# Kernel tuning notes

Measured on AMD Instinct MI355X. Metric: run time of the kernel, lower is better.

## Reference

```python
import jax, jax.numpy as jnp
import numpy as np

N_INPUTS = 1024
N_MIDDLE = 256
N_OUTPUTS = 64
BATCH = 65536


def setup_inputs() -> dict:
    key = jax.random.key(0)
    k_x, k_w1, k_w2 = jax.random.split(key, 3)
    x = jax.random.normal(k_x, (BATCH, N_INPUTS), dtype=jnp.float32)
    # Synapse weights k are initialized with random.random() in [0, 1)
    W1 = jax.random.uniform(k_w1, (N_MIDDLE, N_INPUTS), dtype=jnp.float32)
    W2 = jax.random.uniform(k_w2, (N_OUTPUTS, N_MIDDLE), dtype=jnp.float32)
    # Neuron biases b are initialized to 0.0
    b1 = jnp.zeros((N_MIDDLE,), dtype=jnp.float32)
    b2 = jnp.zeros((N_OUTPUTS,), dtype=jnp.float32)
    return {"x": x, "W1": W1, "b1": b1, "W2": W2, "b2": b2}


def reference(x, W1, b1, W2, b2):
    # Middle RegularNeurons: relu(sum_j k_ij * x_j + b_i)
    h = jax.nn.relu(jnp.einsum('bi,mi->bm', x, W1) + b1)  # [B, n_middle]
    # Output DestinationNeurons: relu(sum_m k_om * h_m + b_o)
    y = jax.nn.relu(jnp.einsum('bm,om->bo', h, W2) + b2)  # [B, n_outputs]
    return y
```

## Files before the change

kernel.cpp:

```cpp
#include <hip/hip_runtime.h>
#include <stdint.h>

#define NIN 1024
#define NMID 256
#define NOUT 64
#define BM 128
#define BK 64
#define NSTEP (NIN / BK)

typedef __attribute__((ext_vector_type(8))) short bf16x8;
typedef __attribute__((ext_vector_type(4))) float fx4;
typedef __attribute__((ext_vector_type(16))) float f32x16;
typedef __attribute__((ext_vector_type(4))) uint32_t u32x4;

#define XS_TILE 16384
#define W1_OFF  32768
#define W1_TILE 32768
#define LDS_SZ  98304

__device__ __forceinline__ uint32_t cvtpk(float lo, float hi) {
  uint32_t r;
  asm("v_cvt_pk_bf16_f32 %0, %1, %2" : "=v"(r) : "v"(lo), "v"(hi));
  return r;
}

__device__ __forceinline__ void gload16(const void* g, void* l) {
  __builtin_amdgcn_global_load_lds(
      (const __attribute__((address_space(1))) uint32_t*)g,
      (__attribute__((address_space(3))) uint32_t*)l, 16, 0, 0);
}

__global__ __launch_bounds__(256) void cvt_weights(
    const float* __restrict__ W1, const float* __restrict__ W2,
    unsigned short* __restrict__ w1b, unsigned short* __restrict__ w2b) {
  int e = (blockIdx.x * 256 + threadIdx.x) << 2;
  const int n1 = NMID * NIN;
  if (e < n1) {
    fx4 v = *(const fx4*)(W1 + e);
    uint2 p;
    p.x = cvtpk(v.x, v.y);
    p.y = cvtpk(v.z, v.w);
    *(uint2*)(w1b + e) = p;
  } else {
    int e2 = e - n1;
    if (e2 < NOUT * NMID) {
      fx4 v = *(const fx4*)(W2 + e2);
      uint2 p;
      p.x = cvtpk(v.x, v.y);
      p.y = cvtpk(v.z, v.w);
      *(uint2*)(w2b + e2) = p;
    }
  }
}

__global__ __launch_bounds__(512, 2) void livenet_main(
    const float* __restrict__ x,
    const unsigned short* __restrict__ w1b,
    const float* __restrict__ b1,
    const unsigned short* __restrict__ w2b,
    const float* __restrict__ b2,
    float* __restrict__ y) {

  extern __shared__ __align__(16) char smem[];

  const int tid = threadIdx.x;
  const int lane = tid & 63;
  const int w = tid >> 6;
  const int wm = w >> 2;
  const int wn = w & 3;
  const int l31 = lane & 31;
  const int lh = lane >> 5;
  const int row0 = blockIdx.x * BM;

  const int xr_row = tid >> 2;
  const int xr_c = tid & 3;
  const float* xbase = x + (size_t)(row0 + xr_row) * NIN + xr_c * 16;
  const int xrx = xr_row & 7;
  const uint32_t xd0 = (uint32_t)(xr_row * 128 + (((2 * xr_c) ^ xrx) << 4));
  const uint32_t xd1 = (uint32_t)(xr_row * 128 + (((2 * xr_c + 1) ^ xrx) << 4));

  uint32_t w1src[4], w1dst[4];
#pragma unroll
  for (int i = 0; i < 4; ++i) {
    uint32_t o = (uint32_t)(i * 8192 + tid * 16);
    uint32_t r = o >> 7;
    uint32_t pc = (o >> 4) & 7u;
    uint32_t j = pc ^ (r & 7u);
    w1src[i] = r * NIN + j * 8u;
    w1dst[i] = o;
  }

  fx4 xl[4];
#define XLOAD(k0)                                     \
  {                                                   \
    const float* p_ = xbase + (k0);                   \
    xl[0] = *(const fx4*)p_;                          \
    xl[1] = *(const fx4*)(p_ + 4);                    \
    xl[2] = *(const fx4*)(p_ + 8);                    \
    xl[3] = *(const fx4*)(p_ + 12);                   \
  }

#define XWRITE(buf)                                                   \
  {                                                                   \
    u32x4 A_ = {cvtpk(xl[0].x, xl[0].y), cvtpk(xl[0].z, xl[0].w),     \
                cvtpk(xl[1].x, xl[1].y), cvtpk(xl[1].z, xl[1].w)};    \
    u32x4 B_ = {cvtpk(xl[2].x, xl[2].y), cvtpk(xl[2].z, xl[2].w),     \
                cvtpk(xl[3].x, xl[3].y), cvtpk(xl[3].z, xl[3].w)};    \
    char* xb_ = smem + (buf) * XS_TILE;                               \
    *(u32x4*)(xb_ + xd0) = A_;                                        \
    *(u32x4*)(xb_ + xd1) = B_;                                        \
  }

#define W1STAGE(buf, k0)                                                      \
  {                                                                           \
    char* wb_ = smem + W1_OFF + (buf) * W1_TILE;                              \
    _Pragma("unroll") for (int i_ = 0; i_ < 4; ++i_)                          \
        gload16(w1b + w1src[i_] + (k0), wb_ + w1dst[i_]);                     \
  }

  f32x16 acc[2][2];
#pragma unroll
  for (int mt = 0; mt < 2; ++mt)
#pragma unroll
    for (int nt = 0; nt < 2; ++nt)
#pragma unroll
      for (int q = 0; q < 16; ++q) acc[mt][nt][q] = 0.f;

  W1STAGE(0, 0);
  XLOAD(0);
  XWRITE(0);
  __syncthreads();

  uint32_t aoff[2], boff[2];
#pragma unroll
  for (int mt = 0; mt < 2; ++mt) {
    uint32_t R = (uint32_t)(wm * 64 + mt * 32 + l31);
    aoff[mt] = R * 128u;
  }
#pragma unroll
  for (int nt = 0; nt < 2; ++nt) {
    uint32_t R = (uint32_t)(wn * 64 + nt * 32 + l31);
    boff[nt] = R * 128u;
  }
  const uint32_t arx0 = (uint32_t)((wm * 64 + l31) & 7);
  const uint32_t brx0 = (uint32_t)((wn * 64 + l31) & 7);

  for (int ks = 0; ks < NSTEP; ++ks) {
    const int cur = ks & 1, nxt = cur ^ 1;
    if (ks + 1 < NSTEP) {
      W1STAGE(nxt, (ks + 1) * BK);
      XLOAD((ks + 1) * BK);
    }

    char* xsb = smem + cur * XS_TILE;
    char* w1sb = smem + W1_OFF + cur * W1_TILE;

    bf16x8 a[2][4], b[2][4];
#pragma unroll
    for (int mt = 0; mt < 2; ++mt) {
      uint32_t rx = arx0;
#pragma unroll
      for (int kk = 0; kk < 4; ++kk)
        a[mt][kk] = *(const bf16x8*)(xsb + aoff[mt] +
                                     ((((uint32_t)(kk * 2 + lh)) ^ rx) << 4));
    }
#pragma unroll
    for (int nt = 0; nt < 2; ++nt) {
      uint32_t rx = brx0;
#pragma unroll
      for (int kk = 0; kk < 4; ++kk)
        b[nt][kk] = *(const bf16x8*)(w1sb + boff[nt] +
                                     ((((uint32_t)(kk * 2 + lh)) ^ rx) << 4));
    }

#pragma unroll
    for (int mt = 0; mt < 2; ++mt)
#pragma unroll
      for (int nt = 0; nt < 2; ++nt)
#pragma unroll
        for (int kk = 0; kk < 4; ++kk)
          acc[mt][nt] = __builtin_amdgcn_mfma_f32_32x32x16_bf16(
              a[mt][kk], b[nt][kk], acc[mt][nt], 0, 0, 0);

    if (ks + 1 < NSTEP) XWRITE(nxt);
    __syncthreads();
  }

  float b1v[2];
#pragma unroll
  for (int nt = 0; nt < 2; ++nt) b1v[nt] = b1[wn * 64 + nt * 32 + l31];

#pragma unroll
  for (int mt = 0; mt < 2; ++mt) {
#pragma unroll
    for (int nt = 0; nt < 2; ++nt) {
      int col = wn * 64 + nt * 32 + l31;
#pragma unroll
      for (int rg = 0; rg < 16; ++rg) {
        int row = wm * 64 + mt * 32 + (rg & 3) + 8 * (rg >> 2) + 4 * lh;
        float v = acc[mt][nt][rg] + b1v[nt];
        v = v > 0.f ? v : 0.f;
        int j = (col >> 3) ^ (row & 31);
        *(unsigned short*)(smem + row * 512 + (j << 4) + (col & 7) * 2) =
            (unsigned short)cvtpk(v, v);
      }
    }
  }
  __syncthreads();

  f32x16 acc2;
#pragma unroll
  for (int q = 0; q < 16; ++q) acc2[q] = 0.f;

  const int r2 = (w >> 1) * 32;
  const int c2 = (w & 1) * 32;
  const int arow = r2 + l31;
  const uint32_t arx = (uint32_t)(arow & 31);
  const unsigned short* w2row = w2b + (size_t)(c2 + l31) * NMID + lh * 8;

#pragma unroll
  for (int kk = 0; kk < 16; ++kk) {
    bf16x8 a2 = *(const bf16x8*)(smem + arow * 512 +
                                 ((((uint32_t)(kk * 2 + lh)) ^ arx) << 4));
    bf16x8 bw = *(const bf16x8*)(w2row + kk * 16);
    acc2 = __builtin_amdgcn_mfma_f32_32x32x16_bf16(a2, bw, acc2, 0, 0, 0);
  }

  float bias2 = b2[c2 + l31];
#pragma unroll
  for (int rg = 0; rg < 16; ++rg) {
    int row = r2 + (rg & 3) + 8 * (rg >> 2) + 4 * lh;
    float v = acc2[rg] + bias2;
    v = v > 0.f ? v : 0.f;
    y[(size_t)(row0 + row) * NOUT + c2 + l31] = v;
  }
}

extern "C" void kernel_launch(void* const* d_in, const int* in_sizes, int n_in,
                              void* d_out, int out_size, void* d_ws, size_t ws_size,
                              hipStream_t stream) {
  const float* x  = (const float*)d_in[0];
  const float* W1 = (const float*)d_in[1];
  const float* b1 = (const float*)d_in[2];
  const float* W2 = (const float*)d_in[3];
  const float* b2 = (const float*)d_in[4];
  float* y = (float*)d_out;

  unsigned short* w1b = (unsigned short*)d_ws;
  unsigned short* w2b = w1b + (size_t)NMID * NIN;

  const int batch = in_sizes[0] / NIN;

  const int tot4 = (NMID * NIN + NOUT * NMID) / 4;
  hipLaunchKernelGGL(cvt_weights, dim3((tot4 + 255) / 256), dim3(256), 0, stream,
                     W1, W2, w1b, w2b);

  static int lds_set = 0;
  if (!lds_set) {
    hipFuncSetAttribute((const void*)livenet_main,
                        hipFuncAttributeMaxDynamicSharedMemorySize, LDS_SZ);
    lds_set = 1;
  }
  hipLaunchKernelGGL(livenet_main, dim3(batch / BM), dim3(512), LDS_SZ, stream,
                     x, w1b, b1, w2b, b2, y);
}
```

Before: 81.86 us.

## Deepen x prefetch with manual vmcnt waits, raw barriers and MFMA priority

Restructures the K-loop so x global loads run two steps ahead in registers while the W1 direct-to-LDS loads run one step ahead. Generic __syncthreads is replaced by explicit s_waitcnt vmcnt/lgkmcnt plus s_barrier and sched_barrier fences, and the loop is peeled into a prologue, 14 steady iterations and an epilogue. s_setprio is raised around the MFMA block to favour matrix issue. The aim is to hide global load latency behind compute and avoid over-conservative waits. The hand-counted vmcnt values depend on load issue order, so a wrong count could race or stall.

```diff
diff --git a/kernel.cpp b/kernel.cpp
--- a/kernel.cpp
+++ b/kernel.cpp
@@ -6,7 +6,6 @@
 #define NOUT 64
 #define BM 128
 #define BK 64
-#define NSTEP (NIN / BK)
 
 typedef __attribute__((ext_vector_type(8))) short bf16x8;
 typedef __attribute__((ext_vector_type(4))) float fx4;
@@ -14,21 +13,26 @@
 typedef __attribute__((ext_vector_type(4))) uint32_t u32x4;
 
 #define XS_TILE 16384
-#define W1_OFF  32768
+#define WOFF    32768
 #define W1_TILE 32768
 #define LDS_SZ  98304
 
-__device__ __forceinline__ uint32_t cvtpk(float lo, float hi) {
+static __device__ __forceinline__ uint32_t cvtpk(float lo, float hi) {
   uint32_t r;
   asm("v_cvt_pk_bf16_f32 %0, %1, %2" : "=v"(r) : "v"(lo), "v"(hi));
   return r;
 }
-
-__device__ __forceinline__ void gload16(const void* g, void* l) {
+static __device__ __forceinline__ void gload16(const void* g, void* l) {
   __builtin_amdgcn_global_load_lds(
       (const __attribute__((address_space(1))) uint32_t*)g,
       (__attribute__((address_space(3))) uint32_t*)l, 16, 0, 0);
 }
+
+#define VMCNT4() asm volatile("s_waitcnt vmcnt(4)" ::: "memory")
+#define VMCNT0() asm volatile("s_waitcnt vmcnt(0)" ::: "memory")
+#define LGKM0()  asm volatile("s_waitcnt lgkmcnt(0)" ::: "memory")
+#define SBAR()   __builtin_amdgcn_s_barrier()
+#define SFENCE() __builtin_amdgcn_sched_barrier(0)
 
 __global__ __launch_bounds__(256) void cvt_weights(
     const float* __restrict__ W1, const float* __restrict__ W2,
@@ -37,17 +41,13 @@
   const int n1 = NMID * NIN;
   if (e < n1) {
     fx4 v = *(const fx4*)(W1 + e);
-    uint2 p;
-    p.x = cvtpk(v.x, v.y);
-    p.y = cvtpk(v.z, v.w);
+    uint2 p; p.x = cvtpk(v.x, v.y); p.y = cvtpk(v.z, v.w);
     *(uint2*)(w1b + e) = p;
   } else {
     int e2 = e - n1;
     if (e2 < NOUT * NMID) {
       fx4 v = *(const fx4*)(W2 + e2);
-      uint2 p;
-      p.x = cvtpk(v.x, v.y);
-      p.y = cvtpk(v.z, v.w);
+      uint2 p; p.x = cvtpk(v.x, v.y); p.y = cvtpk(v.z, v.w);
       *(uint2*)(w2b + e2) = p;
     }
   }
@@ -90,33 +90,27 @@
     w1dst[i] = o;
   }
 
-  fx4 xl[4];
-#define XLOAD(k0)                                     \
-  {                                                   \
-    const float* p_ = xbase + (k0);                   \
-    xl[0] = *(const fx4*)p_;                          \
-    xl[1] = *(const fx4*)(p_ + 4);                    \
-    xl[2] = *(const fx4*)(p_ + 8);                    \
-    xl[3] = *(const fx4*)(p_ + 12);                   \
-  }
-
-#define XWRITE(buf)                                                   \
-  {                                                                   \
-    u32x4 A_ = {cvtpk(xl[0].x, xl[0].y), cvtpk(xl[0].z, xl[0].w),     \
-                cvtpk(xl[1].x, xl[1].y), cvtpk(xl[1].z, xl[1].w)};    \
-    u32x4 B_ = {cvtpk(xl[2].x, xl[2].y), cvtpk(xl[2].z, xl[2].w),     \
-                cvtpk(xl[3].x, xl[3].y), cvtpk(xl[3].z, xl[3].w)};    \
-    char* xb_ = smem + (buf) * XS_TILE;                               \
+  fx4 xr[4];
+#define XLOAD(k0)                               \
+  { const float* p_ = xbase + (k0);             \
+    xr[0] = *(const fx4*)p_;                    \
+    xr[1] = *(const fx4*)(p_ + 4);              \
+    xr[2] = *(const fx4*)(p_ + 8);              \
+    xr[3] = *(const fx4*)(p_ + 12); }
+
+#define XWRITE(pbuf)                                                  \
+  { u32x4 A_ = {cvtpk(xr[0].x, xr[0].y), cvtpk(xr[0].z, xr[0].w),     \
+                cvtpk(xr[1].x, xr[1].y), cvtpk(xr[1].z, xr[1].w)};    \
+    u32x4 B_ = {cvtpk(xr[2].x, xr[2].y), cvtpk(xr[2].z, xr[2].w),     \
+                cvtpk(xr[3].x, xr[3].y), cvtpk(xr[3].z, xr[3].w)};    \
+    char* xb_ = smem + (pbuf) * XS_TILE;                              \
     *(u32x4*)(xb_ + xd0) = A_;                                        \
-    *(u32x4*)(xb_ + xd1) = B_;                                        \
-  }
-
-#define W1STAGE(buf, k0)                                                      \
-  {                                                                           \
-    char* wb_ = smem + W1_OFF + (buf) * W1_TILE;                              \
-    _Pragma("unroll") for (int i_ = 0; i_ < 4; ++i_)                          \
-        gload16(w1b + w1src[i_] + (k0), wb_ + w1dst[i_]);                     \
-  }
+    *(u32x4*)(xb_ + xd1) = B_; }
+
+#define W1STAGE(pbuf, k0)                                             \
+  { char* wb_ = smem + WOFF + (pbuf) * W1_TILE;                       \
+    _Pragma("unroll") for (int i_ = 0; i_ < 4; ++i_)                  \
+      gload16(w1b + w1src[i_] + (k0), wb_ + w1dst[i_]); }
 
   f32x16 acc[2][2];
 #pragma unroll
@@ -126,65 +120,80 @@
 #pragma unroll
       for (int q = 0; q < 16; ++q) acc[mt][nt][q] = 0.f;
 
-  W1STAGE(0, 0);
-  XLOAD(0);
-  XWRITE(0);
-  __syncthreads();
-
   uint32_t aoff[2], boff[2];
 #pragma unroll
-  for (int mt = 0; mt < 2; ++mt) {
-    uint32_t R = (uint32_t)(wm * 64 + mt * 32 + l31);
-    aoff[mt] = R * 128u;
-  }
-#pragma unroll
-  for (int nt = 0; nt < 2; ++nt) {
-    uint32_t R = (uint32_t)(wn * 64 + nt * 32 + l31);
-    boff[nt] = R * 128u;
-  }
+  for (int mt = 0; mt < 2; ++mt)
+    aoff[mt] = (uint32_t)(wm * 64 + mt * 32 + l31) * 128u;
+#pragma unroll
+  for (int nt = 0; nt < 2; ++nt)
+    boff[nt] = (uint32_t)(wn * 64 + nt * 32 + l31) * 128u;
   const uint32_t arx0 = (uint32_t)((wm * 64 + l31) & 7);
   const uint32_t brx0 = (uint32_t)((wn * 64 + l31) & 7);
 
-  for (int ks = 0; ks < NSTEP; ++ks) {
-    const int cur = ks & 1, nxt = cur ^ 1;
-    if (ks + 1 < NSTEP) {
-      W1STAGE(nxt, (ks + 1) * BK);
-      XLOAD((ks + 1) * BK);
-    }
-
-    char* xsb = smem + cur * XS_TILE;
-    char* w1sb = smem + W1_OFF + cur * W1_TILE;
-
-    bf16x8 a[2][4], b[2][4];
-#pragma unroll
-    for (int mt = 0; mt < 2; ++mt) {
-      uint32_t rx = arx0;
-#pragma unroll
-      for (int kk = 0; kk < 4; ++kk)
-        a[mt][kk] = *(const bf16x8*)(xsb + aoff[mt] +
-                                     ((((uint32_t)(kk * 2 + lh)) ^ rx) << 4));
-    }
-#pragma unroll
-    for (int nt = 0; nt < 2; ++nt) {
-      uint32_t rx = brx0;
-#pragma unroll
-      for (int kk = 0; kk < 4; ++kk)
-        b[nt][kk] = *(const bf16x8*)(w1sb + boff[nt] +
-                                     ((((uint32_t)(kk * 2 + lh)) ^ rx) << 4));
-    }
-
-#pragma unroll
-    for (int mt = 0; mt < 2; ++mt)
-#pragma unroll
-      for (int nt = 0; nt < 2; ++nt)
-#pragma unroll
-        for (int kk = 0; kk < 4; ++kk)
-          acc[mt][nt] = __builtin_amdgcn_mfma_f32_32x32x16_bf16(
-              a[mt][kk], b[nt][kk], acc[mt][nt], 0, 0, 0);
-
-    if (ks + 1 < NSTEP) XWRITE(nxt);
-    __syncthreads();
-  }
+#define STEP_COMPUTE(xb, wb)                                              \
+  { bf16x8 a[2][4], b[2][4];                                              \
+    _Pragma("unroll") for (int mt = 0; mt < 2; ++mt)                      \
+      _Pragma("unroll") for (int kk = 0; kk < 4; ++kk)                    \
+        a[mt][kk] = *(const bf16x8*)((xb) + aoff[mt] +                    \
+                     ((((uint32_t)(kk * 2 + lh)) ^ arx0) << 4));          \
+    _Pragma("unroll") for (int nt = 0; nt < 2; ++nt)                      \
+      _Pragma("unroll") for (int kk = 0; kk < 4; ++kk)                    \
+        b[nt][kk] = *(const bf16x8*)((wb) + boff[nt] +                    \
+                     ((((uint32_t)(kk * 2 + lh)) ^ brx0) << 4));          \
+    __builtin_amdgcn_s_setprio(1);                                        \
+    _Pragma("unroll") for (int mt = 0; mt < 2; ++mt)                      \
+      _Pragma("unroll") for (int nt = 0; nt < 2; ++nt)                    \
+        _Pragma("unroll") for (int kk = 0; kk < 4; ++kk)                  \
+          acc[mt][nt] = __builtin_amdgcn_mfma_f32_32x32x16_bf16(          \
+              a[mt][kk], b[nt][kk], acc[mt][nt], 0, 0, 0);                \
+    __builtin_amdgcn_s_setprio(0); }
+
+  XLOAD(0);
+  W1STAGE(0, 0);
+  VMCNT4();
+  SFENCE();
+  XWRITE(0);
+  XLOAD(BK);
+  VMCNT4();
+  LGKM0();
+  SBAR();
+  SFENCE();
+
+  for (int t = 0; t < 14; ++t) {
+    const int pc = t & 1, pn = pc ^ 1;
+    char* xb = smem + pc * XS_TILE;
+    char* wb = smem + WOFF + pc * W1_TILE;
+    W1STAGE(pn, (t + 1) * BK);
+    STEP_COMPUTE(xb, wb);
+    VMCNT4();
+    SFENCE();
+    XWRITE(pn);
+    XLOAD((t + 2) * BK);
+    VMCNT4();
+    LGKM0();
+    SBAR();
+    SFENCE();
+  }
+
+  {
+    char* xb = smem + 0 * XS_TILE;
+    char* wb = smem + WOFF + 0 * W1_TILE;
+    W1STAGE(1, 15 * BK);
+    STEP_COMPUTE(xb, wb);
+    VMCNT4();
+    SFENCE();
+    XWRITE(1);
+    VMCNT0();
+    LGKM0();
+    SBAR();
+    SFENCE();
+  }
+  {
+    char* xb = smem + 1 * XS_TILE;
+    char* wb = smem + WOFF + 1 * W1_TILE;
+    STEP_COMPUTE(xb, wb);
+  }
+  __syncthreads();
 
   float b1v[2];
 #pragma unroll
```

New measurement: 77.50 us. 5.3% less time.

## Stream fp32 x tiles to LDS directly and read W1 fragments from global

Applied to the files above, without the earlier changes.

The weight-conversion kernel now writes W1 in a fragment-major bf16 layout, so each wave reads its B fragments straight from global/L2 instead of staging W1 through LDS. The x tile is copied as raw fp32 into LDS with async global_load_lds and converted to bf16 at fragment-read time, which removes the register round-trip and LDS write path for x. LDS use drops from 96 KB to 64 KB and launch bounds ask for more resident blocks; MFMA issue is bracketed with s_setprio. In exchange, LDS traffic for x doubles because it is stored as fp32, and the conversions move into the inner loop.

```diff
diff --git a/kernel.cpp b/kernel.cpp
--- a/kernel.cpp
+++ b/kernel.cpp
@@ -6,25 +6,23 @@
 #define NOUT 64
 #define BM 128
 #define BK 64
-#define NSTEP (NIN / BK)
 
 typedef __attribute__((ext_vector_type(8))) short bf16x8;
 typedef __attribute__((ext_vector_type(4))) float fx4;
 typedef __attribute__((ext_vector_type(16))) float f32x16;
 typedef __attribute__((ext_vector_type(4))) uint32_t u32x4;
 
-#define XS_TILE 16384
-#define W1_OFF  32768
-#define W1_TILE 32768
-#define LDS_SZ  98304
-
-__device__ __forceinline__ uint32_t cvtpk(float lo, float hi) {
+#define XS_TILE 32768
+#define LDS_SZ  65536
+
+union FragU { bf16x8 v; uint32_t u[4]; };
+
+static __device__ __forceinline__ uint32_t cvtpk(float lo, float hi) {
   uint32_t r;
   asm("v_cvt_pk_bf16_f32 %0, %1, %2" : "=v"(r) : "v"(lo), "v"(hi));
   return r;
 }
-
-__device__ __forceinline__ void gload16(const void* g, void* l) {
+static __device__ __forceinline__ void gload16(const void* g, void* l) {
   __builtin_amdgcn_global_load_lds(
       (const __attribute__((address_space(1))) uint32_t*)g,
       (__attribute__((address_space(3))) uint32_t*)l, 16, 0, 0);
@@ -32,30 +30,31 @@
 
 __global__ __launch_bounds__(256) void cvt_weights(
     const float* __restrict__ W1, const float* __restrict__ W2,
-    unsigned short* __restrict__ w1b, unsigned short* __restrict__ w2b) {
-  int e = (blockIdx.x * 256 + threadIdx.x) << 2;
-  const int n1 = NMID * NIN;
-  if (e < n1) {
-    fx4 v = *(const fx4*)(W1 + e);
-    uint2 p;
-    p.x = cvtpk(v.x, v.y);
-    p.y = cvtpk(v.z, v.w);
-    *(uint2*)(w1b + e) = p;
+    unsigned short* __restrict__ w1f, unsigned short* __restrict__ w2b) {
+  int gid = blockIdx.x * 256 + threadIdx.x;
+  if (gid < 32768) {
+    int r = gid & 31;
+    int kb = (gid >> 5) & 127;
+    int c = gid >> 12;
+    const float* s = W1 + (size_t)(c * 32 + r) * NIN + kb * 8;
+    fx4 v0 = *(const fx4*)s;
+    fx4 v1 = *(const fx4*)(s + 4);
+    u32x4 o = {cvtpk(v0.x, v0.y), cvtpk(v0.z, v0.w),
+               cvtpk(v1.x, v1.y), cvtpk(v1.z, v1.w)};
+    *(u32x4*)(w1f + (size_t)gid * 8) = o;
   } else {
-    int e2 = e - n1;
+    int e2 = (gid - 32768) << 2;
     if (e2 < NOUT * NMID) {
       fx4 v = *(const fx4*)(W2 + e2);
-      uint2 p;
-      p.x = cvtpk(v.x, v.y);
-      p.y = cvtpk(v.z, v.w);
+      uint2 p; p.x = cvtpk(v.x, v.y); p.y = cvtpk(v.z, v.w);
       *(uint2*)(w2b + e2) = p;
     }
   }
 }
 
-__global__ __launch_bounds__(512, 2) void livenet_main(
+__global__ __launch_bounds__(512, 4) void livenet_main(
     const float* __restrict__ x,
-    const unsigned short* __restrict__ w1b,
+    const unsigned short* __restrict__ w1f,
     const float* __restrict__ b1,
     const unsigned short* __restrict__ w2b,
     const float* __restrict__ b2,
@@ -69,54 +68,25 @@
   const int wm = w >> 2;
   const int wn = w & 3;
   const int l31 = lane & 31;
+  const int l15 = lane & 15;
   const int lh = lane >> 5;
   const int row0 = blockIdx.x * BM;
 
-  const int xr_row = tid >> 2;
-  const int xr_c = tid & 3;
-  const float* xbase = x + (size_t)(row0 + xr_row) * NIN + xr_c * 16;
-  const int xrx = xr_row & 7;
-  const uint32_t xd0 = (uint32_t)(xr_row * 128 + (((2 * xr_c) ^ xrx) << 4));
-  const uint32_t xd1 = (uint32_t)(xr_row * 128 + (((2 * xr_c + 1) ^ xrx) << 4));
-
-  uint32_t w1src[4], w1dst[4];
+  uint32_t xsrc[4], xdst[4];
 #pragma unroll
   for (int i = 0; i < 4; ++i) {
     uint32_t o = (uint32_t)(i * 8192 + tid * 16);
-    uint32_t r = o >> 7;
-    uint32_t pc = (o >> 4) & 7u;
-    uint32_t j = pc ^ (r & 7u);
-    w1src[i] = r * NIN + j * 8u;
-    w1dst[i] = o;
-  }
-
-  fx4 xl[4];
-#define XLOAD(k0)                                     \
-  {                                                   \
-    const float* p_ = xbase + (k0);                   \
-    xl[0] = *(const fx4*)p_;                          \
-    xl[1] = *(const fx4*)(p_ + 4);                    \
-    xl[2] = *(const fx4*)(p_ + 8);                    \
-    xl[3] = *(const fx4*)(p_ + 12);                   \
-  }
-
-#define XWRITE(buf)                                                   \
-  {                                                                   \
-    u32x4 A_ = {cvtpk(xl[0].x, xl[0].y), cvtpk(xl[0].z, xl[0].w),     \
-                cvtpk(xl[1].x, xl[1].y), cvtpk(xl[1].z, xl[1].w)};    \
-    u32x4 B_ = {cvtpk(xl[2].x, xl[2].y), cvtpk(xl[2].z, xl[2].w),     \
-                cvtpk(xl[3].x, xl[3].y), cvtpk(xl[3].z, xl[3].w)};    \
-    char* xb_ = smem + (buf) * XS_TILE;                               \
-    *(u32x4*)(xb_ + xd0) = A_;                                        \
-    *(u32x4*)(xb_ + xd1) = B_;                                        \
-  }
-
-#define W1STAGE(buf, k0)                                                      \
-  {                                                                           \
-    char* wb_ = smem + W1_OFF + (buf) * W1_TILE;                              \
-    _Pragma("unroll") for (int i_ = 0; i_ < 4; ++i_)                          \
-        gload16(w1b + w1src[i_] + (k0), wb_ + w1dst[i_]);                     \
-  }
+    uint32_t r = o >> 8;
+    uint32_t pc = (o >> 4) & 15u;
+    uint32_t j = pc ^ (r & 15u);
+    xsrc[i] = (uint32_t)(row0 + (int)r) * NIN + j * 4u;
+    xdst[i] = o;
+  }
+
+#define XSTAGE(pbuf, k0)                                        \
+  { char* xb_ = smem + (pbuf) * XS_TILE;                        \
+    _Pragma("unroll") for (int i_ = 0; i_ < 4; ++i_)            \
+      gload16(x + xsrc[i_] + (k0), xb_ + xdst[i_]); }
 
   f32x16 acc[2][2];
 #pragma unroll
@@ -126,63 +96,54 @@
 #pragma unroll
       for (int q = 0; q < 16; ++q) acc[mt][nt][q] = 0.f;
 
-  W1STAGE(0, 0);
-  XLOAD(0);
-  XWRITE(0);
+  const unsigned short* wf0 = w1f + ((size_t)(wn * 2 + 0) * 4096 + l31) * 8;
+  const unsigned short* wf1 = w1f + ((size_t)(wn * 2 + 1) * 4096 + l31) * 8;
+
+  const uint32_t ar0 = (uint32_t)(wm * 64 + l31) * 256u;
+  const uint32_t ar1 = (uint32_t)(wm * 64 + 32 + l31) * 256u;
+
+  XSTAGE(0, 0);
   __syncthreads();
 
-  uint32_t aoff[2], boff[2];
-#pragma unroll
-  for (int mt = 0; mt < 2; ++mt) {
-    uint32_t R = (uint32_t)(wm * 64 + mt * 32 + l31);
-    aoff[mt] = R * 128u;
-  }
-#pragma unroll
-  for (int nt = 0; nt < 2; ++nt) {
-    uint32_t R = (uint32_t)(wn * 64 + nt * 32 + l31);
-    boff[nt] = R * 128u;
-  }
-  const uint32_t arx0 = (uint32_t)((wm * 64 + l31) & 7);
-  const uint32_t brx0 = (uint32_t)((wn * 64 + l31) & 7);
-
-  for (int ks = 0; ks < NSTEP; ++ks) {
-    const int cur = ks & 1, nxt = cur ^ 1;
-    if (ks + 1 < NSTEP) {
-      W1STAGE(nxt, (ks + 1) * BK);
-      XLOAD((ks + 1) * BK);
-    }
-
-    char* xsb = smem + cur * XS_TILE;
-    char* w1sb = smem + W1_OFF + cur * W1_TILE;
-
-    bf16x8 a[2][4], b[2][4];
-#pragma unroll
-    for (int mt = 0; mt < 2; ++mt) {
-      uint32_t rx = arx0;
-#pragma unroll
-      for (int kk = 0; kk < 4; ++kk)
-        a[mt][kk] = *(const bf16x8*)(xsb + aoff[mt] +
-                                     ((((uint32_t)(kk * 2 + lh)) ^ rx) << 4));
-    }
-#pragma unroll
-    for (int nt = 0; nt < 2; ++nt) {
-      uint32_t rx = brx0;
-#pragma unroll
-      for (int kk = 0; kk < 4; ++kk)
-        b[nt][kk] = *(const bf16x8*)(w1sb + boff[nt] +
-                                     ((((uint32_t)(kk * 2 + lh)) ^ rx) << 4));
-    }
-
-#pragma unroll
-    for (int mt = 0; mt < 2; ++mt)
-#pragma unroll
-      for (int nt = 0; nt < 2; ++nt)
-#pragma unroll
-        for (int kk = 0; kk < 4; ++kk)
-          acc[mt][nt] = __builtin_amdgcn_mfma_f32_32x32x16_bf16(
-              a[mt][kk], b[nt][kk], acc[mt][nt], 0, 0, 0);
-
-    if (ks + 1 < NSTEP) XWRITE(nxt);
+  for (int t = 0; t < 16; ++t) {
+    const int pc = t & 1;
+    const char* xb = smem + pc * XS_TILE;
+
+    bf16x8 bfr[2][4];
+#pragma unroll
+    for (int kk = 0; kk < 4; ++kk) {
+      uint32_t kb = (uint32_t)(t * 8 + kk * 2 + lh);
+      bfr[0][kk] = *(const bf16x8*)(wf0 + kb * 256u);
+      bfr[1][kk] = *(const bf16x8*)(wf1 + kb * 256u);
+    }
+
+    if (t < 15) XSTAGE(pc ^ 1, (t + 1) * BK);
+
+#pragma unroll
+    for (int kk = 0; kk < 4; ++kk) {
+      bf16x8 a0, a1;
+      {
+        uint32_t j0 = (uint32_t)(kk * 4 + lh * 2);
+        fx4 va = *(const fx4*)(xb + ar0 + ((j0 ^ (uint32_t)l15) << 4));
+        fx4 vb = *(const fx4*)(xb + ar0 + (((j0 + 1) ^ (uint32_t)l15) << 4));
+        FragU f;
+        f.u[0] = cvtpk(va.x, va.y); f.u[1] = cvtpk(va.z, va.w);
+        f.u[2] = cvtpk(vb.x, vb.y); f.u[3] = cvtpk(vb.z, vb.w);
+        a0 = f.v;
+        fx4 vc = *(const fx4*)(xb + ar1 + ((j0 ^ (uint32_t)l15) << 4));
+        fx4 vd = *(const fx4*)(xb + ar1 + (((j0 + 1) ^ (uint32_t)l15) << 4));
+        FragU g;
+        g.u[0] = cvtpk(vc.x, vc.y); g.u[1] = cvtpk(vc.z, vc.w);
+        g.u[2] = cvtpk(vd.x, vd.y); g.u[3] = cvtpk(vd.z, vd.w);
+        a1 = g.v;
+      }
+      __builtin_amdgcn_s_setprio(1);
+      acc[0][0] = __builtin_amdgcn_mfma_f32_32x32x16_bf16(a0, bfr[0][kk], acc[0][0], 0, 0, 0);
+      acc[0][1] = __builtin_amdgcn_mfma_f32_32x32x16_bf16(a0, bfr[1][kk], acc[0][1], 0, 0, 0);
+      acc[1][0] = __builtin_amdgcn_mfma_f32_32x32x16_bf16(a1, bfr[0][kk], acc[1][0], 0, 0, 0);
+      acc[1][1] = __builtin_amdgcn_mfma_f32_32x32x16_bf16(a1, bfr[1][kk], acc[1][1], 0, 0, 0);
+      __builtin_amdgcn_s_setprio(0);
+    }
     __syncthreads();
   }
 
@@ -246,14 +207,13 @@
   const float* b2 = (const float*)d_in[4];
   float* y = (float*)d_out;
 
-  unsigned short* w1b = (unsigned short*)d_ws;
-  unsigned short* w2b = w1b + (size_t)NMID * NIN;
+  unsigned short* w1f = (unsigned short*)d_ws;
+  unsigned short* w2b = w1f + (size_t)NMID * NIN;
 
   const int batch = in_sizes[0] / NIN;
 
-  const int tot4 = (NMID * NIN + NOUT * NMID) / 4;
-  hipLaunchKernelGGL(cvt_weights, dim3((tot4 + 255) / 256), dim3(256), 0, stream,
-                     W1, W2, w1b, w2b);
+  hipLaunchKernelGGL(cvt_weights, dim3(144), dim3(256), 0, stream,
+                     W1, W2, w1f, w2b);
 
   static int lds_set = 0;
   if (!lds_set) {
@@ -262,5 +222,5 @@
     lds_set = 1;
   }
   hipLaunchKernelGGL(livenet_main, dim3(batch / BM), dim3(512), LDS_SZ, stream,
-                     x, w1b, b1, w2b, b2, y);
-}
+                     x, w1f, b1, w2b, b2, y);
+}
```

New measurement: 89.19 us. +9.0%, slower.
